# Optimization experiments

Hardware: AMD Instinct MI355X
Metric: run time of the kernel (lower is better)

The kernel has to match this reference:

```python
import jax, jax.numpy as jnp
import numpy as np

EPS = 1e-5  # torch LayerNorm default


def setup_inputs() -> dict:
    key = jax.random.key(0)
    ks = jax.random.split(key, 4)
    B, S, D = 8, 1024, 768
    return {
        "q": jax.random.normal(ks[0], (B, S, D), dtype=jnp.float32),
        "k": jax.random.normal(ks[1], (B, S, D), dtype=jnp.float32),
        "v": jax.random.normal(ks[2], (B, S, D), dtype=jnp.float32),
        "W": jax.random.normal(ks[3], (D, D), dtype=jnp.float32) * (1.0 / np.sqrt(D)),
        "gamma": jnp.ones((D,), dtype=jnp.float32),
        "beta": jnp.zeros((D,), dtype=jnp.float32),
        "n_heads": 12,
    }


def reference(q, k, v, W, gamma, beta, n_heads):
    # Shapes: q,k,v [B,S,D]; W [D,D] (torch Linear weight, y = x @ W.T)
    B, S, D = q.shape
    Dh = D // n_heads

    proj = lambda x: jax.nn.relu(x @ W.T)
    q1, k1, v1 = proj(q), proj(k), proj(v)

    # chunk(dim=2) + cat(dim=0) == reshape to per-head [B,S,H,Dh]
    split = lambda x: x.reshape(B, S, n_heads, Dh)
    qh, kh, vh = split(q1), split(k1), split(v1)

    scale = 1.0 / (Dh ** 0.5)
    scores = jnp.einsum("bqhd,bkhd->bhqk", qh, kh) * scale  # [B,H,S,S]
    attn = jax.nn.softmax(scores, axis=-1)  # dropout is identity in eval mode
    out = jnp.einsum("bhqk,bkhd->bqhd", attn, vh).reshape(B, S, D)

    # `outputs += outputs + q` in torch -> outputs = 2*outputs + q
    out = 2.0 * out + q

    mu = jnp.mean(out, axis=-1, keepdims=True)
    var = jnp.var(out, axis=-1, keepdims=True)
    return (out - mu) / jnp.sqrt(var + EPS) * gamma + beta
```

## Files before the change

### kernel.cpp

```cpp
#include <hip/hip_runtime.h>
#include <hip/hip_bf16.h>

#define B_  8
#define S_  1024
#define D_  768
#define H_  12
#define DH_ 64

typedef __attribute__((ext_vector_type(8))) short bf16x8;
typedef __attribute__((ext_vector_type(4))) float f32x4;
typedef __attribute__((ext_vector_type(16))) float f32x16;

__device__ inline short f2bf(float f) {
    unsigned u = __builtin_bit_cast(unsigned, f);
    u = (u + 0x7fffu + ((u >> 16) & 1u)) >> 16;
    return (short)u;
}
__device__ inline float exp2_fast(float x) {
    float r; asm("v_exp_f32 %0, %1" : "=v"(r) : "v"(x)); return r;
}
__device__ inline unsigned cvt_pk_bf16(float lo, float hi) {
    unsigned r; asm("v_cvt_pk_bf16_f32 %0, %1, %2" : "=v"(r) : "v"(lo), "v"(hi)); return r;
}
__device__ inline float rcp_fast(float x) {
    float r; asm("v_rcp_f32 %0, %1" : "=v"(r) : "v"(x)); return r;
}
__device__ inline void plswap(unsigned& a, unsigned& b) {
    auto r = __builtin_amdgcn_permlane32_swap(a, b, false, false);
    a = r[0]; b = r[1];
}
__device__ inline float2 xhalves(float x) {
    unsigned u = __builtin_bit_cast(unsigned, x);
    auto r = __builtin_amdgcn_permlane32_swap(u, u, false, false);
    return make_float2(__builtin_bit_cast(float, r[0]),
                       __builtin_bit_cast(float, r[1]));
}
__device__ inline void gl_lds16(const void* gsrc, char* ldst) {
    __builtin_amdgcn_global_load_lds(
        (const __attribute__((address_space(1))) unsigned int*)gsrc,
        (__attribute__((address_space(3))) unsigned int*)ldst,
        16, 0, 0);
}

__global__ __launch_bounds__(256) void convw_kernel(
    const float* __restrict__ W, short* __restrict__ Wb)
{
    int i = (blockIdx.x * 256 + threadIdx.x) * 8;
    f32x4 a = *(const f32x4*)(W + i);
    f32x4 b = *(const f32x4*)(W + i + 4);
    uint4 pk;
    pk.x = cvt_pk_bf16(a[0], a[1]); pk.y = cvt_pk_bf16(a[2], a[3]);
    pk.z = cvt_pk_bf16(b[0], b[1]); pk.w = cvt_pk_bf16(b[2], b[3]);
    *(uint4*)(Wb + i) = pk;
}

__global__ __launch_bounds__(512) void proj_kernel(
    const float* __restrict__ q, const float* __restrict__ k,
    const float* __restrict__ v, const short* __restrict__ Wb,
    short* __restrict__ q1, short* __restrict__ k1, short* __restrict__ v1t)
{
    __shared__ __align__(16) char lds[98304];

    int p  = blockIdx.x;
    int L  = (p & 7) * 32 + (p >> 3);
    int mt = L >> 1, nb = L & 1;
    int m0 = mt << 6;
    int n0 = nb * 384;

    int tid = threadIdx.x, lane = tid & 63, w = tid >> 6;
    int l15 = lane & 15, g = lane >> 4;

    int xrow = w * 8 + (lane >> 3), xc = lane & 7;
    size_t xoff = (size_t)(m0 + xrow) * D_ + ((xc ^ (xrow & 7)) << 2);
    const float* xs0 = q + xoff;
    const float* xs1 = k + xoff;
    const float* xs2 = v + xoff;
    int wrow0 = w * 48 + (lane >> 2), wc = lane & 3;
    int wrow1 = wrow0 + 16, wrow2 = wrow0 + 32;
    const short* wsrc0 = Wb + (size_t)(n0 + wrow0) * D_ + ((wc ^ ((wrow0 >> 1) & 3)) << 3);
    const short* wsrc1 = Wb + (size_t)(n0 + wrow1) * D_ + ((wc ^ ((wrow1 >> 1) & 3)) << 3);
    const short* wsrc2 = Wb + (size_t)(n0 + wrow2) * D_ + ((wc ^ ((wrow2 >> 1) & 3)) << 3);

#define ISSUE(s_, b_) do { int _ko = (s_) * 32; \
        char* _bb = lds + (b_) * 49152; \
        gl_lds16(xs0 + _ko, _bb + w * 1024); \
        gl_lds16(xs1 + _ko, _bb + 8192 + w * 1024); \
        gl_lds16(xs2 + _ko, _bb + 16384 + w * 1024); \
        gl_lds16(wsrc0 + _ko, _bb + 24576 + w * 3072); \
        gl_lds16(wsrc1 + _ko, _bb + 24576 + w * 3072 + 1024); \
        gl_lds16(wsrc2 + _ko, _bb + 24576 + w * 3072 + 2048); \
    } while (0)

    f32x4 acc[3][4][3];
    #pragma unroll
    for (int t = 0; t < 3; t++)
        #pragma unroll
        for (int m = 0; m < 4; m++)
            #pragma unroll
            for (int n = 0; n < 3; n++) acc[t][m][n] = (f32x4){0.f, 0.f, 0.f, 0.f};

    ISSUE(0, 0);
    for (int s = 0; s < 24; ++s) {
        __builtin_amdgcn_s_barrier();
        asm volatile("" ::: "memory");
        if (s + 1 < 24) {
            ISSUE(s + 1, (s + 1) & 1);
            asm volatile("s_waitcnt vmcnt(6)" ::: "memory");
        } else {
            asm volatile("s_waitcnt vmcnt(0)" ::: "memory");
        }
        __builtin_amdgcn_s_barrier();
        asm volatile("" ::: "memory");

        const char* bb = lds + (s & 1) * 49152;
        const char* Wp = bb + 24576;
        bf16x8 bfv[3];
        #pragma unroll
        for (int n = 0; n < 3; n++) {
            int r = w * 48 + n * 16 + l15;
            bfv[n] = *(const bf16x8*)(Wp + r * 64 + ((g ^ ((r >> 1) & 3)) << 4));
        }
        #pragma unroll
        for (int t = 0; t < 3; t++) {
            const char* Xb = bb + t * 8192;
            bf16x8 af[4];
            #pragma unroll
            for (int m = 0; m < 4; m++) {
                int r = m * 16 + l15;
                const char* rp = Xb + r * 128;
                f32x4 lo = *(const f32x4*)(rp + (((2 * g)     ^ (r & 7)) << 4));
                f32x4 hi = *(const f32x4*)(rp + (((2 * g + 1) ^ (r & 7)) << 4));
                uint4 pk;
                pk.x = cvt_pk_bf16(lo[0], lo[1]); pk.y = cvt_pk_bf16(lo[2], lo[3]);
                pk.z = cvt_pk_bf16(hi[0], hi[1]); pk.w = cvt_pk_bf16(hi[2], hi[3]);
                af[m] = __builtin_bit_cast(bf16x8, pk);
            }
            __builtin_amdgcn_s_setprio(1);
            #pragma unroll
            for (int m = 0; m < 4; m++)
                #pragma unroll
                for (int n = 0; n < 3; n++)
                    acc[t][m][n] = __builtin_amdgcn_mfma_f32_16x16x32_bf16(
                        af[m], bfv[n], acc[t][m][n], 0, 0, 0);
            __builtin_amdgcn_s_setprio(0);
        }
    }
#undef ISSUE

    int bb2 = m0 >> 10;
    #pragma unroll
    for (int t = 0; t < 3; t++) {
        __syncthreads();
        const float sc1 = (t == 1) ? 0.18033688011112793f : 1.0f;
        #pragma unroll
        for (int m = 0; m < 4; m++)
            #pragma unroll
            for (int n = 0; n < 3; n++)
                #pragma unroll
                for (int r = 0; r < 4; r++) {
                    int row = m * 16 + g * 4 + r;
                    int col = w * 48 + n * 16 + l15;
                    short vv = f2bf(fmaxf(acc[t][m][n][r], 0.f) * sc1);
                    if (t == 2)
                        *(short*)(lds + col * 128 + (((row >> 3) ^ (col & 7)) << 4)
                                  + ((row & 7) << 1)) = vv;
                    else
                        *(short*)(lds + row * 768 + (((col >> 3) ^ (row & 7)) << 4)
                                  + ((col & 7) << 1)) = vv;
                }
        __syncthreads();
        if (t == 2) {
            #pragma unroll
            for (int j = 0; j < 6; j++) {
                int c = tid * 6 + j;
                int vr = c >> 3, ch = c & 7;
                bf16x8 val = *(const bf16x8*)(lds + vr * 128 + ((ch ^ (vr & 7)) << 4));
                int gc = n0 + vr, h = gc >> 6, dh = gc & 63;
                *(bf16x8*)(v1t + (((size_t)bb2 * H_ + h) * DH_ + dh) * S_
                           + (m0 & 1023) + ch * 8) = val;
            }
        } else {
            short* dst0 = t ? k1 : q1;
            #pragma unroll
            for (int j = 0; j < 6; j++) {
                int c = tid * 6 + j;
                int row = c / 48, ch = c % 48;
                bf16x8 val = *(const bf16x8*)(lds + row * 768 + ((ch ^ (row & 7)) << 4));
                int m = m0 + row, ss = m & 1023;
                int gc = n0 + ch * 8, h = gc >> 6, dh = gc & 63;
                *(bf16x8*)(dst0 + (((size_t)bb2 * H_ + h) * S_ + ss) * DH_ + dh) = val;
            }
        }
    }
}

__global__ __launch_bounds__(256, 3) void attn_kernel(
    const short* __restrict__ q1, const short* __restrict__ k1,
    const short* __restrict__ v1t, float* __restrict__ out)
{
    __shared__ short Klds[2][4096];
    __shared__ short Vlds[2][4096];
    __shared__ float lsum_lds[4][32];

    int d    = blockIdx.x;
    int head = (d & 7) + ((d >> 6) << 3);
    int qi   = (d >> 3) & 7;
    int bb   = head / H_, hh = head % H_;

    int tid = threadIdx.x, lane = tid & 63, w = tid >> 6;
    int l31 = lane & 31, hi = lane >> 5;
    int qbase = (qi * 4 + w) * 32;

    const short* Qp = q1  + (size_t)head * S_ * DH_;
    const short* Kp = k1  + (size_t)head * S_ * DH_;
    const short* Vp = v1t + (size_t)head * DH_ * S_;

    int sr = tid >> 2, sc = tid & 3;
    int swz0 = sr * 128 + ((sc       ^ (sr & 7)) << 4);
    int swz1 = sr * 128 + (((sc + 4) ^ (sr & 7)) << 4);

    bf16x8 stK0, stK1, stV0, stV1;

#define LOADST(kvb) do { \
        const short* _kg = Kp + (size_t)((kvb) + sr) * DH_; \
        const short* _vg = Vp + (size_t)sr * S_ + (kvb); \
        stK0 = *(const bf16x8*)(_kg + sc * 8); \
        stK1 = *(const bf16x8*)(_kg + (sc + 4) * 8); \
        stV0 = *(const bf16x8*)(_vg + sc * 8); \
        stV1 = *(const bf16x8*)(_vg + (sc + 4) * 8); \
    } while (0)
#define WRITEST(buf) do { \
        char* _kb = (char*)&Klds[buf][0]; \
        char* _vb = (char*)&Vlds[buf][0]; \
        *(bf16x8*)(_kb + swz0) = stK0; \
        *(bf16x8*)(_kb + swz1) = stK1; \
        *(bf16x8*)(_vb + swz0) = stV0; \
        *(bf16x8*)(_vb + swz1) = stV1; \
    } while (0)

    bf16x8 qf[4];
    #pragma unroll
    for (int kb = 0; kb < 4; kb++)
        qf[kb] = *(const bf16x8*)(Qp + (size_t)(qbase + l31) * DH_ + kb * 16 + hi * 8);

    f32x16 o0, o1;
    #pragma unroll
    for (int r = 0; r < 16; r++) { o0[r] = 0.f; o1[r] = 0.f; }
    float mreg = -1e30f, lsum = 0.f;

    int xk = l31 & 7;

    auto subtile = [&](int cur, int j) {
        const char* Kt = (const char*)&Klds[cur][0];
        const char* Vt = (const char*)&Vlds[cur][0];
        int rK = (32 * j + l31) * 128;
        bf16x8 kf0 = *(const bf16x8*)(Kt + rK + (((0 + hi) ^ xk) << 4));
        bf16x8 kf1 = *(const bf16x8*)(Kt + rK + (((2 + hi) ^ xk) << 4));
        bf16x8 kf2 = *(const bf16x8*)(Kt + rK + (((4 + hi) ^ xk) << 4));
        bf16x8 kf3 = *(const bf16x8*)(Kt + rK + (((6 + hi) ^ xk) << 4));
        int rV0 = l31 * 128, rV1 = (32 + l31) * 128;
        int s0 = ((4 * j + hi) ^ xk) << 4, s1 = ((4 * j + 2 + hi) ^ xk) << 4;
        bf16x8 vf00 = *(const bf16x8*)(Vt + rV0 + s0);
        bf16x8 vf01 = *(const bf16x8*)(Vt + rV0 + s1);
        bf16x8 vf10 = *(const bf16x8*)(Vt + rV1 + s0);
        bf16x8 vf11 = *(const bf16x8*)(Vt + rV1 + s1);

        f32x16 s;
        #pragma unroll
        for (int r = 0; r < 16; r++) s[r] = 0.f;
        __builtin_amdgcn_s_setprio(1);
        s = __builtin_amdgcn_mfma_f32_32x32x16_bf16(kf0, qf[0], s, 0, 0, 0);
        s = __builtin_amdgcn_mfma_f32_32x32x16_bf16(kf1, qf[1], s, 0, 0, 0);
        s = __builtin_amdgcn_mfma_f32_32x32x16_bf16(kf2, qf[2], s, 0, 0, 0);
        s = __builtin_amdgcn_mfma_f32_32x32x16_bf16(kf3, qf[3], s, 0, 0, 0);
        __builtin_amdgcn_s_setprio(0);

        float t0 = fmaxf(s[0], s[1]),   t1 = fmaxf(s[2], s[3]);
        float t2 = fmaxf(s[4], s[5]),   t3 = fmaxf(s[6], s[7]);
        float t4 = fmaxf(s[8], s[9]),   t5 = fmaxf(s[10], s[11]);
        float t6 = fmaxf(s[12], s[13]), t7 = fmaxf(s[14], s[15]);
        float u0 = fmaxf(t0, t1), u1 = fmaxf(t2, t3);
        float u2 = fmaxf(t4, t5), u3 = fmaxf(t6, t7);
        float pmax = fmaxf(fmaxf(u0, u1), fmaxf(u2, u3));
        float2 ph = xhalves(pmax);
        pmax = fmaxf(ph.x, ph.y);

        if (!__all(pmax <= mreg + 8.f)) {
            float mn = fmaxf(mreg, pmax);
            float sc_ = exp2_fast(mreg - mn);
            mreg = mn; lsum *= sc_;
            if (hi == 0) lsum_lds[w][l31] = sc_;
            asm volatile("s_waitcnt lgkmcnt(0)" ::: "memory");
            #pragma unroll
            for (int r = 0; r < 16; r++) {
                int crow = (r & 3) + ((r >> 2) << 3) + (hi << 2);
                float srw = lsum_lds[w][crow];
                o0[r] *= srw; o1[r] *= srw;
            }
        }

        #pragma unroll
        for (int r = 0; r < 16; r++) s[r] = exp2_fast(s[r] - mreg);

        float a0 = s[0] + s[1],   a1 = s[2] + s[3];
        float a2 = s[4] + s[5],   a3 = s[6] + s[7];
        float a4 = s[8] + s[9],   a5 = s[10] + s[11];
        float a6 = s[12] + s[13], a7 = s[14] + s[15];
        float rsum = ((a0 + a1) + (a2 + a3)) + ((a4 + a5) + (a6 + a7));
        float2 rh = xhalves(rsum);
        lsum += rh.x + rh.y;

        unsigned c0 = cvt_pk_bf16(s[0], s[1]);
        unsigned c1 = cvt_pk_bf16(s[2], s[3]);
        unsigned c2 = cvt_pk_bf16(s[4], s[5]);
        unsigned c3 = cvt_pk_bf16(s[6], s[7]);
        unsigned c4 = cvt_pk_bf16(s[8], s[9]);
        unsigned c5 = cvt_pk_bf16(s[10], s[11]);
        unsigned c6 = cvt_pk_bf16(s[12], s[13]);
        unsigned c7 = cvt_pk_bf16(s[14], s[15]);
        plswap(c0, c2);
        plswap(c1, c3);
        plswap(c4, c6);
        plswap(c5, c7);

        union U { unsigned u[4]; bf16x8 v; };
        U f0, f1;
        f0.u[0] = c0; f0.u[1] = c1; f0.u[2] = c2; f0.u[3] = c3;
        f1.u[0] = c4; f1.u[1] = c5; f1.u[2] = c6; f1.u[3] = c7;

        __builtin_amdgcn_s_setprio(1);
        o0 = __builtin_amdgcn_mfma_f32_32x32x16_bf16(f0.v, vf00, o0, 0, 0, 0);
        o0 = __builtin_amdgcn_mfma_f32_32x32x16_bf16(f1.v, vf01, o0, 0, 0, 0);
        o1 = __builtin_amdgcn_mfma_f32_32x32x16_bf16(f0.v, vf10, o1, 0, 0, 0);
        o1 = __builtin_amdgcn_mfma_f32_32x32x16_bf16(f1.v, vf11, o1, 0, 0, 0);
        __builtin_amdgcn_s_setprio(0);
    };

    LOADST(0);
    WRITEST(0);
    LOADST(64);
    asm volatile("s_waitcnt lgkmcnt(0)" ::: "memory");
    __builtin_amdgcn_s_barrier();
    asm volatile("" ::: "memory");

    int cur = 0;
    for (int t = 0; t < 16; t++) {
        if (t < 15) {
            WRITEST(cur ^ 1);
            if (t < 14) LOADST((t + 2) * 64);
        }
        subtile(cur, 0);
        subtile(cur, 1);
        if (t < 15) {
            asm volatile("" ::: "memory");
            asm volatile("s_waitcnt lgkmcnt(0)" ::: "memory");
            __builtin_amdgcn_s_barrier();
            asm volatile("" ::: "memory");
        }
        cur ^= 1;
    }
#undef LOADST
#undef WRITEST

    if (hi == 0) lsum_lds[w][l31] = lsum;
    asm volatile("s_waitcnt lgkmcnt(0)" ::: "memory");
    #pragma unroll
    for (int r = 0; r < 16; r++) {
        int crow = (r & 3) + ((r >> 2) << 3) + (hi << 2);
        float inv = rcp_fast(lsum_lds[w][crow]);
        float* op = out + ((size_t)(bb * S_ + qbase + crow)) * D_ + hh * DH_ + l31;
        op[0]  = o0[r] * inv;
        op[32] = o1[r] * inv;
    }
}

__global__ __launch_bounds__(192) void ln_kernel(
    const float* __restrict__ qin, const float* __restrict__ gamma,
    const float* __restrict__ beta, float* __restrict__ out)
{
    int row = blockIdx.x;
    int tid = threadIdx.x;
    size_t base = (size_t)row * D_ + tid * 4;

    f32x4 o  = *(const f32x4*)(out + base);
    f32x4 qv = *(const f32x4*)(qin + base);
    f32x4 x;
    float sum = 0.f, sq = 0.f;
    #pragma unroll
    for (int i = 0; i < 4; i++) {
        x[i] = 2.f * o[i] + qv[i];
        sum += x[i];
        sq  += x[i] * x[i];
    }
    #pragma unroll
    for (int msk = 1; msk < 64; msk <<= 1) {
        sum += __shfl_xor(sum, msk);
        sq  += __shfl_xor(sq, msk);
    }
    __shared__ float s1[3], s2[3];
    if ((tid & 63) == 0) { s1[tid >> 6] = sum; s2[tid >> 6] = sq; }
    __syncthreads();
    sum = s1[0] + s1[1] + s1[2];
    sq  = s2[0] + s2[1] + s2[2];
    float mu   = sum * (1.f / D_);
    float var  = sq * (1.f / D_) - mu * mu;
    float rstd = rsqrtf(var + 1e-5f);
    f32x4 g = *(const f32x4*)(gamma + tid * 4);
    f32x4 b = *(const f32x4*)(beta + tid * 4);
    f32x4 y;
    #pragma unroll
    for (int i = 0; i < 4; i++)
        y[i] = (x[i] - mu) * rstd * g[i] + b[i];
    *(f32x4*)(out + base) = y;
}

extern "C" void kernel_launch(void* const* d_in, const int* in_sizes, int n_in,
                              void* d_out, int out_size, void* d_ws, size_t ws_size,
                              hipStream_t stream)
{
    const float* q     = (const float*)d_in[0];
    const float* k     = (const float*)d_in[1];
    const float* v     = (const float*)d_in[2];
    const float* W     = (const float*)d_in[3];
    const float* gamma = (const float*)d_in[4];
    const float* beta  = (const float*)d_in[5];

    size_t per = (size_t)B_ * H_ * S_ * DH_;
    short* q1  = (short*)d_ws;
    short* k1  = q1 + per;
    short* v1t = k1 + per;
    short* Wb  = v1t + per;
    float* out = (float*)d_out;

    convw_kernel<<<dim3(288), dim3(256), 0, stream>>>(W, Wb);
    proj_kernel<<<dim3(256), dim3(512), 0, stream>>>(q, k, v, Wb, q1, k1, v1t);
    attn_kernel<<<dim3(768), dim3(256), 0, stream>>>(q1, k1, v1t, out);
    ln_kernel<<<dim3(B_ * S_), dim3(192), 0, stream>>>(q, gamma, beta, out);
}
```

Baseline: 109.9 us.

## Split projection GEMM into 192-column tiles with 256-thread blocks, doubling grid

```diff
diff --git a/kernel.cpp b/kernel.cpp
--- a/kernel.cpp
+++ b/kernel.cpp
@@ -54,41 +54,43 @@
     *(uint4*)(Wb + i) = pk;
 }
 
-__global__ __launch_bounds__(512) void proj_kernel(
+__global__ __launch_bounds__(256) void proj_kernel(
     const float* __restrict__ q, const float* __restrict__ k,
     const float* __restrict__ v, const short* __restrict__ Wb,
     short* __restrict__ q1, short* __restrict__ k1, short* __restrict__ v1t)
 {
-    __shared__ __align__(16) char lds[98304];
+    __shared__ __align__(16) char lds[73728];
 
     int p  = blockIdx.x;
-    int L  = (p & 7) * 32 + (p >> 3);
-    int mt = L >> 1, nb = L & 1;
+    int L  = (p & 7) * 64 + (p >> 3);
+    int mt = L >> 2, nq = L & 3;
     int m0 = mt << 6;
-    int n0 = nb * 384;
+    int n0 = nq * 192;
 
     int tid = threadIdx.x, lane = tid & 63, w = tid >> 6;
     int l15 = lane & 15, g = lane >> 4;
 
-    int xrow = w * 8 + (lane >> 3), xc = lane & 7;
-    size_t xoff = (size_t)(m0 + xrow) * D_ + ((xc ^ (xrow & 7)) << 2);
-    const float* xs0 = q + xoff;
-    const float* xs1 = k + xoff;
-    const float* xs2 = v + xoff;
-    int wrow0 = w * 48 + (lane >> 2), wc = lane & 3;
-    int wrow1 = wrow0 + 16, wrow2 = wrow0 + 32;
-    const short* wsrc0 = Wb + (size_t)(n0 + wrow0) * D_ + ((wc ^ ((wrow0 >> 1) & 3)) << 3);
-    const short* wsrc1 = Wb + (size_t)(n0 + wrow1) * D_ + ((wc ^ ((wrow1 >> 1) & 3)) << 3);
-    const short* wsrc2 = Wb + (size_t)(n0 + wrow2) * D_ + ((wc ^ ((wrow2 >> 1) & 3)) << 3);
+    int xr0 = w * 16 + (lane >> 3), xr1 = xr0 + 8;
+    int xc  = lane & 7;
+    size_t xo0 = (size_t)(m0 + xr0) * D_ + ((xc ^ (xr0 & 7)) << 2);
+    size_t xo1 = (size_t)(m0 + xr1) * D_ + ((xc ^ (xr1 & 7)) << 2);
+    int wr0 = w * 48 + (lane >> 2), wr1 = wr0 + 16, wr2 = wr0 + 32;
+    int wc  = lane & 3;
+    const short* ws0 = Wb + (size_t)(n0 + wr0) * D_ + ((wc ^ ((wr0 >> 1) & 3)) << 3);
+    const short* ws1 = Wb + (size_t)(n0 + wr1) * D_ + ((wc ^ ((wr1 >> 1) & 3)) << 3);
+    const short* ws2 = Wb + (size_t)(n0 + wr2) * D_ + ((wc ^ ((wr2 >> 1) & 3)) << 3);
 
 #define ISSUE(s_, b_) do { int _ko = (s_) * 32; \
-        char* _bb = lds + (b_) * 49152; \
-        gl_lds16(xs0 + _ko, _bb + w * 1024); \
-        gl_lds16(xs1 + _ko, _bb + 8192 + w * 1024); \
-        gl_lds16(xs2 + _ko, _bb + 16384 + w * 1024); \
-        gl_lds16(wsrc0 + _ko, _bb + 24576 + w * 3072); \
-        gl_lds16(wsrc1 + _ko, _bb + 24576 + w * 3072 + 1024); \
-        gl_lds16(wsrc2 + _ko, _bb + 24576 + w * 3072 + 2048); \
+        char* _bb = lds + (b_) * 36864; \
+        gl_lds16(q + xo0 + _ko, _bb + (w * 16) * 128); \
+        gl_lds16(q + xo1 + _ko, _bb + (w * 16 + 8) * 128); \
+        gl_lds16(k + xo0 + _ko, _bb + 8192 + (w * 16) * 128); \
+        gl_lds16(k + xo1 + _ko, _bb + 8192 + (w * 16 + 8) * 128); \
+        gl_lds16(v + xo0 + _ko, _bb + 16384 + (w * 16) * 128); \
+        gl_lds16(v + xo1 + _ko, _bb + 16384 + (w * 16 + 8) * 128); \
+        gl_lds16(ws0 + _ko, _bb + 24576 + (w * 48) * 64); \
+        gl_lds16(ws1 + _ko, _bb + 24576 + (w * 48 + 16) * 64); \
+        gl_lds16(ws2 + _ko, _bb + 24576 + (w * 48 + 32) * 64); \
     } while (0)
 
     f32x4 acc[3][4][3];
@@ -105,14 +107,14 @@
         asm volatile("" ::: "memory");
         if (s + 1 < 24) {
             ISSUE(s + 1, (s + 1) & 1);
-            asm volatile("s_waitcnt vmcnt(6)" ::: "memory");
+            asm volatile("s_waitcnt vmcnt(9)" ::: "memory");
         } else {
             asm volatile("s_waitcnt vmcnt(0)" ::: "memory");
         }
         __builtin_amdgcn_s_barrier();
         asm volatile("" ::: "memory");
 
-        const char* bb = lds + (s & 1) * 49152;
+        const char* bb = lds + (s & 1) * 36864;
         const char* Wp = bb + 24576;
         bf16x8 bfv[3];
         #pragma unroll
@@ -165,7 +167,7 @@
                         *(short*)(lds + col * 128 + (((row >> 3) ^ (col & 7)) << 4)
                                   + ((row & 7) << 1)) = vv;
                     else
-                        *(short*)(lds + row * 768 + (((col >> 3) ^ (row & 7)) << 4)
+                        *(short*)(lds + row * 384 + (((col >> 3) ^ (row & 7)) << 4)
                                   + ((col & 7) << 1)) = vv;
                 }
         __syncthreads();
@@ -184,8 +186,8 @@
             #pragma unroll
             for (int j = 0; j < 6; j++) {
                 int c = tid * 6 + j;
-                int row = c / 48, ch = c % 48;
-                bf16x8 val = *(const bf16x8*)(lds + row * 768 + ((ch ^ (row & 7)) << 4));
+                int row = c / 24, ch = c % 24;
+                bf16x8 val = *(const bf16x8*)(lds + row * 384 + ((ch ^ (row & 7)) << 4));
                 int m = m0 + row, ss = m & 1023;
                 int gc = n0 + ch * 8, h = gc >> 6, dh = gc & 63;
                 *(bf16x8*)(dst0 + (((size_t)bb2 * H_ + h) * S_ + ss) * DH_ + dh) = val;
@@ -433,7 +435,7 @@
     float* out = (float*)d_out;
 
     convw_kernel<<<dim3(288), dim3(256), 0, stream>>>(W, Wb);
-    proj_kernel<<<dim3(256), dim3(512), 0, stream>>>(q, k, v, Wb, q1, k1, v1t);
+    proj_kernel<<<dim3(512), dim3(256), 0, stream>>>(q, k, v, Wb, q1, k1, v1t);
     attn_kernel<<<dim3(768), dim3(256), 0, stream>>>(q1, k1, v1t, out);
     ln_kernel<<<dim3(B_ * S_), dim3(192), 0, stream>>>(q, gamma, beta, out);
 }
```

Measured after the change: 128.7 us. 1.17x slower.
